# Kernel tuning notes

Measured on AMD Instinct MI355X. Metric: run time of the kernel, lower is better.

Reference implementation:

```python
import jax, jax.numpy as jnp
import numpy as np
import math

B, S, D = 1, 4096, 512
H, KVH, DH = 8, 4, 64
DH2 = DH // 2
M = int(math.isqrt(S))           # product-key grid side, S == M*M
K = 8                            # top_k
ROPE_BASE = 10000.0


def rope_cos_sin(seq_len, dh, base):
    inv_freq = 1.0 / (base ** (jnp.arange(0, dh, 2, dtype=jnp.float32) / dh))
    t = jnp.arange(seq_len, dtype=jnp.float32)
    freqs = jnp.outer(t, inv_freq)                      # (S, dh/2)
    emb = jnp.concatenate([freqs, freqs], axis=-1)      # (S, dh)
    return jnp.cos(emb), jnp.sin(emb)


def apply_rope(x, cos, sin):
    # x: (B, H, S, dh); half-split rotation (llama-style)
    dh2 = x.shape[-1] // 2
    rot = jnp.concatenate([-x[..., dh2:], x[..., :dh2]], axis=-1)
    return x * cos + rot * sin


def setup_inputs() -> dict:
    key = jax.random.key(0)
    ks = jax.random.split(key, 5)
    s = 0.02
    x = jax.random.normal(ks[0], (B, S, D), dtype=jnp.float32)
    Wq = jax.random.normal(ks[1], (H * DH, D), dtype=jnp.float32) * s
    Wk = jax.random.normal(ks[2], (KVH * DH, D), dtype=jnp.float32) * s
    Wv = jax.random.normal(ks[3], (KVH * DH, D), dtype=jnp.float32) * s
    Wo = jax.random.normal(ks[4], (D, H * DH), dtype=jnp.float32) * s
    return {"x": x, "Wq": Wq, "Wk": Wk, "Wv": Wv, "Wo": Wo}


def reference(x, Wq, Wk, Wv, Wo):
    b, s, d = x.shape
    cos, sin = rope_cos_sin(s, DH, ROPE_BASE)
    q = (x @ Wq.T).reshape(b, s, H, DH).transpose(0, 2, 1, 3)      # (B,H,S,DH)
    k = (x @ Wk.T).reshape(b, s, KVH, DH).transpose(0, 2, 1, 3)    # (B,KVH,S,DH)
    v = (x @ Wv.T).reshape(b, s, KVH, DH).transpose(0, 2, 1, 3)
    q = apply_rope(q, cos, sin)
    k = apply_rope(k, cos, sin)
    rep = H // KVH                                                 # GQA repeat_kv
    k = jnp.repeat(k, rep, axis=1)                                 # (B,H,S,DH)
    v = jnp.repeat(v, rep, axis=1)

    # factorized product keys: sum over grid rows / cols
    kg = k.reshape(b, H, M, M, DH)
    k1 = kg[..., :DH2].sum(axis=-2)                                # (B,H,M,DH2)
    k2 = kg[..., DH2:].sum(axis=-3)                                # (B,H,M,DH2)
    q1, q2 = q[..., :DH2], q[..., DH2:]

    def topk_sel(qh, kh):  # qh: (S,DH2), kh: (M,DH2)
        scores = qh @ kh.T                                         # (S,M)
        _, idx = jax.lax.top_k(scores, K)                          # (S,K)
        return kh[idx], idx                                        # (S,K,DH2), (S,K)

    sel2 = jax.vmap(jax.vmap(topk_sel))
    k1v, i1 = sel2(q1, k1)                                         # (B,H,S,K,DH2)
    k2v, i2 = sel2(q2, k2)

    # cross-product candidates: (B,H,S,K,K,DH) -> (B,H,S,K*K,DH)
    c1 = jnp.broadcast_to(k1v[:, :, :, :, None, :], (b, H, s, K, K, DH2))
    c2 = jnp.broadcast_to(k2v[:, :, :, None, :, :], (b, H, s, K, K, DH2))
    cand = jnp.concatenate([c1, c2], axis=-1).reshape(b, H, s, K * K, DH)

    scores_final = jnp.einsum('bhsd,bhscd->bhsc', q, cand)         # (B,H,S,K*K)
    _, sel = jax.lax.top_k(scores_final, K)                        # (B,H,S,K)
    final_k = jnp.take_along_axis(cand, sel[..., None], axis=3)    # (B,H,S,K,DH)

    row = jnp.take_along_axis(i1, sel // K, axis=3)
    col = jnp.take_along_axis(i2, sel % K, axis=3)
    v_idx = row * M + col                                          # (B,H,S,K)
    final_v = jax.vmap(jax.vmap(lambda vb, ib: vb[ib]))(v, v_idx)  # (B,H,S,K,DH)

    attn = jax.nn.softmax(
        jnp.einsum('bhsd,bhskd->bhsk', q, final_k) / math.sqrt(DH), axis=-1)
    o = jnp.einsum('bhsk,bhskd->bhsd', attn, final_v)              # (B,H,S,DH)
    o = o.transpose(0, 2, 1, 3).reshape(b, s, H * DH)
    return o @ Wo.T
```

## Files before the change

kernel.cpp:

```cpp
#include <hip/hip_runtime.h>
#include <math.h>


static constexpr size_t OFF_P1   = 0;
static constexpr size_t OFF_P2   = 4194304;
static constexpr size_t OFF_Q    = 8388608;
static constexpr size_t OFF_K    = 10485760;
static constexpr size_t OFF_V    = 11534336;
static constexpr size_t OFF_COS  = 12582912;
static constexpr size_t OFF_SIN  = 12713984;
static constexpr size_t OFF_K1   = 12845056;
static constexpr size_t OFF_K2   = 12853248;
static constexpr size_t OFF_O    = 12861440;
static constexpr size_t OFF_W    = 14958592;
static constexpr size_t OFF_PACK = 15482880;

#define LDB 132

__device__ __forceinline__ float rdlane_f(float v, int lane) {
  return __int_as_float(__builtin_amdgcn_readlane(__float_as_int(v), lane));
}

__global__ __launch_bounds__(256) void freq_table_kernel(float* __restrict__ cosT,
    float* __restrict__ sinT) {
  int idx = blockIdx.x * 256 + threadIdx.x;
  int s = idx >> 5;
  int dp = idx & 31;
  double e = (double)dp * (1.0 / 32.0);
  float pf = (float)pow(10000.0, e);
  float invf = 1.0f / pf;
  float argf = __fmul_rn((float)s, invf);
  cosT[idx] = (float)cos((double)argf);
  sinT[idx] = (float)sin((double)argf);
}

__global__ __launch_bounds__(256) void gemm128_panel(const float* __restrict__ A,
    const float* __restrict__ B, float* __restrict__ C1, float* __restrict__ C2,
    int N, int ksplit) {
  __shared__ float As[16 * LDB];
  __shared__ float Bs[16 * LDB];
  const int tid = threadIdx.x;
  const int z = blockIdx.z;
  const int k0 = z ? ksplit : 0;
  const int k1 = z ? 512 : ksplit;
  float* __restrict__ C = z ? C2 : C1;
  const int bm = blockIdx.y, bn = blockIdx.x;
  const int lrow = tid >> 1;
  const int lko = (tid & 1) << 3;
  const int ty = tid >> 4;
  const int tx = tid & 15;
  const float* Ap = A + (size_t)(bm * 128 + lrow) * 512 + lko;
  const float* Bp = B + (size_t)(bn * 128 + lrow) * 512 + lko;
  float acc[8][8] = {{0.f}};
  float4 a0 = *(const float4*)(Ap + k0);
  float4 a1 = *(const float4*)(Ap + k0 + 4);
  float4 b0 = *(const float4*)(Bp + k0);
  float4 b1 = *(const float4*)(Bp + k0 + 4);
  for (int kt = k0; kt < k1; kt += 16) {
    __syncthreads();
    As[(lko + 0) * LDB + lrow] = a0.x;
    As[(lko + 1) * LDB + lrow] = a0.y;
    As[(lko + 2) * LDB + lrow] = a0.z;
    As[(lko + 3) * LDB + lrow] = a0.w;
    As[(lko + 4) * LDB + lrow] = a1.x;
    As[(lko + 5) * LDB + lrow] = a1.y;
    As[(lko + 6) * LDB + lrow] = a1.z;
    As[(lko + 7) * LDB + lrow] = a1.w;
    Bs[(lko + 0) * LDB + lrow] = b0.x;
    Bs[(lko + 1) * LDB + lrow] = b0.y;
    Bs[(lko + 2) * LDB + lrow] = b0.z;
    Bs[(lko + 3) * LDB + lrow] = b0.w;
    Bs[(lko + 4) * LDB + lrow] = b1.x;
    Bs[(lko + 5) * LDB + lrow] = b1.y;
    Bs[(lko + 6) * LDB + lrow] = b1.z;
    Bs[(lko + 7) * LDB + lrow] = b1.w;
    __syncthreads();
    if (kt + 16 < k1) {
      a0 = *(const float4*)(Ap + kt + 16);
      a1 = *(const float4*)(Ap + kt + 20);
      b0 = *(const float4*)(Bp + kt + 16);
      b1 = *(const float4*)(Bp + kt + 20);
    }
    #pragma unroll
    for (int k = 0; k < 16; ++k) {
      float4 al = *(const float4*)(&As[k * LDB + (ty << 2)]);
      float4 ah = *(const float4*)(&As[k * LDB + 64 + (ty << 2)]);
      float4 bl = *(const float4*)(&Bs[k * LDB + (tx << 2)]);
      float4 bh = *(const float4*)(&Bs[k * LDB + 64 + (tx << 2)]);
      float af[8] = {al.x, al.y, al.z, al.w, ah.x, ah.y, ah.z, ah.w};
      float bf[8] = {bl.x, bl.y, bl.z, bl.w, bh.x, bh.y, bh.z, bh.w};
      #pragma unroll
      for (int i2 = 0; i2 < 8; ++i2)
        #pragma unroll
        for (int j2 = 0; j2 < 8; ++j2)
          acc[i2][j2] = fmaf(af[i2], bf[j2], acc[i2][j2]);
    }
  }
  #pragma unroll
  for (int i2 = 0; i2 < 8; ++i2) {
    int row = bm * 128 + ((i2 < 4) ? (ty << 2) + i2 : 64 + (ty << 2) + i2 - 4);
    float* Cp = C + (size_t)row * N + bn * 128;
    *(float4*)(Cp + (tx << 2))      = make_float4(acc[i2][0], acc[i2][1], acc[i2][2], acc[i2][3]);
    *(float4*)(Cp + 64 + (tx << 2)) = make_float4(acc[i2][4], acc[i2][5], acc[i2][6], acc[i2][7]);
  }
}

__global__ __launch_bounds__(256) void combine_kernel(const float* __restrict__ p1,
    const float* __restrict__ p2, float* __restrict__ out) {
  int i = blockIdx.x * 256 + threadIdx.x;
  out[i] = __fadd_rn(p1[i], p2[i]);
}

__global__ __launch_bounds__(256) void rope_reshape_kernel(const float* __restrict__ p1,
    const float* __restrict__ p2, const float* __restrict__ cosT,
    const float* __restrict__ sinT, float* __restrict__ qb,
    float* __restrict__ kb, float* __restrict__ vb) {
  int idx = blockIdx.x * 256 + threadIdx.x;
  int s = idx >> 10;
  int n = idx & 1023;
  float val = __fadd_rn(p1[idx], p2[idx]);
  int d = n & 63;
  if (n < 768) {
    int dp = d & 31;
    float cs = cosT[(s << 5) + dp];
    float sn = sinT[(s << 5) + dp];
    int npart = (n - d) + ((d < 32) ? d + 32 : d - 32);
    int pidx = (s << 10) + npart;
    float partner = __fadd_rn(p1[pidx], p2[pidx]);
    float rot = (d < 32) ? -partner : partner;
    float out = __fadd_rn(__fmul_rn(val, cs), __fmul_rn(rot, sn));
    if (n < 512) {
      int h = n >> 6;
      qb[((size_t)(h * 4096 + s) << 6) + d] = out;
    } else {
      int kvh = (n - 512) >> 6;
      kb[((size_t)(kvh * 4096 + s) << 6) + d] = out;
    }
  } else {
    int kvh = (n - 768) >> 6;
    vb[((size_t)(kvh * 4096 + s) << 6) + d] = val;
  }
}

__global__ __launch_bounds__(256) void k12_np_kernel(const float* __restrict__ kb,
    float* __restrict__ k1t, float* __restrict__ k2t) {
  int id = blockIdx.x * 256 + threadIdx.x;
  int which = id >> 13;
  int rem = id & 8191;
  int kvh = rem >> 11;
  int rem2 = rem & 2047;
  int i = rem2 >> 5;
  int d = rem2 & 31;
  const float* base = kb + ((size_t)(kvh * 4096) << 6);
  if (which == 0) {
    float acc = base[((size_t)(i * 64) << 6) + d];
    for (int c = 1; c < 64; ++c)
      acc = __fadd_rn(acc, base[((size_t)(i * 64 + c) << 6) + d]);
    k1t[(kvh * 64 + i) * 32 + d] = acc;
  } else {
    float acc = base[((size_t)i << 6) + d + 32];
    for (int r = 1; r < 64; ++r)
      acc = __fadd_rn(acc, base[((size_t)(r * 64 + i) << 6) + d + 32]);
    k2t[(kvh * 64 + i) * 32 + d] = acc;
  }
}

__global__ __launch_bounds__(256) void stage1_scoresT_kernel(
    const float* __restrict__ qb, const float* __restrict__ k1t,
    const float* __restrict__ k2t, float* __restrict__ scT) {
  __shared__ float qs[64 * 68];
  __shared__ float kd[32 * 132];
  const int t = threadIdx.x;
  const int h = blockIdx.y;
  const int s0 = blockIdx.x * 64;
  const int kvh = h >> 1;
  #pragma unroll
  for (int i = 0; i < 16; ++i) {
    int j = t + i * 256;
    int ss = j >> 6, d = j & 63;
    qs[d * 68 + ss] = qb[((size_t)(h * 4096 + s0 + ss) << 6) + d];
  }
  #pragma unroll
  for (int i = 0; i < 8; ++i) {
    int j = t + i * 256;
    int r = j >> 5, d = j & 31;
    kd[d * 132 + r]      = k1t[(kvh * 64 + r) * 32 + d];
    kd[d * 132 + 64 + r] = k2t[(kvh * 64 + r) * 32 + d];
  }
  __syncthreads();
  const int ty = t >> 4;
  const int tx = t & 15;
  float acc1[4][4] = {{0.f}};
  float acc2[4][4] = {{0.f}};
  #pragma unroll
  for (int dp = 0; dp < 32; ++dp) {
    float4 kv1 = *(const float4*)&kd[dp * 132 + (ty << 2)];
    float4 kv2 = *(const float4*)&kd[dp * 132 + 64 + (ty << 2)];
    float4 q1 = *(const float4*)&qs[dp * 68 + (tx << 2)];
    float4 q2 = *(const float4*)&qs[(32 + dp) * 68 + (tx << 2)];
    float k1f[4] = {kv1.x, kv1.y, kv1.z, kv1.w};
    float k2f[4] = {kv2.x, kv2.y, kv2.z, kv2.w};
    float q1f[4] = {q1.x, q1.y, q1.z, q1.w};
    float q2f[4] = {q2.x, q2.y, q2.z, q2.w};
    #pragma unroll
    for (int i2 = 0; i2 < 4; ++i2)
      #pragma unroll
      for (int j2 = 0; j2 < 4; ++j2) {
        acc1[i2][j2] = fmaf(k1f[i2], q1f[j2], acc1[i2][j2]);
        acc2[i2][j2] = fmaf(k2f[i2], q2f[j2], acc2[i2][j2]);
      }
  }
  float* base = scT + (size_t)h * 524288 + s0 + (tx << 2);
  #pragma unroll
  for (int i2 = 0; i2 < 4; ++i2) {
    *(float4*)(base + (size_t)((ty << 2) + i2) * 4096) =
        make_float4(acc1[i2][0], acc1[i2][1], acc1[i2][2], acc1[i2][3]);
    *(float4*)(base + (size_t)(64 + (ty << 2) + i2) * 4096) =
        make_float4(acc2[i2][0], acc2[i2][1], acc2[i2][2], acc2[i2][3]);
  }
}

__global__ __launch_bounds__(64) void sel1_kernel(const float* __restrict__ scT,
    ulonglong2* __restrict__ packs) {
  const int w = blockIdx.x * 64 + threadIdx.x;
  const int h = w >> 12;
  const int s = w & 4095;
  const float* base = scT + (size_t)h * 524288 + s;
  unsigned long long pk[2];
  #pragma unroll
  for (int set = 0; set < 2; ++set) {
    const float* p = base + (size_t)set * 64 * 4096;
    float top[8];
    int idx[8];
    #pragma unroll
    for (int t = 0; t < 8; ++t) { top[t] = -INFINITY; idx[t] = 0; }
    #pragma unroll
    for (int r = 0; r < 64; ++r) {
      float v = p[(size_t)r * 4096];
      int i = r;
      #pragma unroll
      for (int j = 0; j < 8; ++j) {
        bool gt = v > top[j];
        float tv = top[j]; int ti = idx[j];
        top[j] = gt ? v : tv;
        idx[j] = gt ? i : ti;
        v = gt ? tv : v;
        i = gt ? ti : i;
      }
    }
    unsigned long long pp = 0;
    #pragma unroll
    for (int t = 0; t < 8; ++t) pp |= (unsigned long long)idx[t] << (6 * t);
    pk[set] = pp;
  }
  ulonglong2 out;
  out.x = pk[0];
  out.y = pk[1];
  packs[w] = out;
}

__device__ __forceinline__ void bitonic64_val_desc(float& v, int lane) {
  #pragma unroll
  for (int k = 2; k <= 64; k <<= 1) {
    #pragma unroll
    for (int j = k >> 1; j >= 1; j >>= 1) {
      float ov = __shfl_xor(v, j, 64);
      bool up = ((lane & k) == 0) == ((lane & j) == 0);
      float mx = fmaxf(v, ov), mn = fminf(v, ov);
      v = up ? mx : mn;
    }
  }
}

__global__ __launch_bounds__(256) void attn_sel2_kernel(
    const ulonglong2* __restrict__ packs, const float* __restrict__ qb,
    const float* __restrict__ vb, const float* __restrict__ k1t,
    const float* __restrict__ k2t, float* __restrict__ ob) {
  const int lane = threadIdx.x & 63;
  const int w = blockIdx.x * 4 + (threadIdx.x >> 6);
  const int h = w >> 12;
  const int s = w & 4095;
  const int kvh = h >> 1;
  ulonglong2 pk = packs[w];
  const unsigned long long pack1 = pk.x, pack2 = pk.y;
  const float qv = qb[((size_t)w << 6) + lane];

  int r1 = (int)((pack1 >> (6 * (lane >> 3))) & 63);
  int r2 = (int)((pack2 >> (6 * (lane & 7))) & 63);
  const float* k1p = k1t + (size_t)(kvh * 64 + r1) * 32;
  const float* k2p = k2t + (size_t)(kvh * 64 + r2) * 32;
  float c = 0.f;
  #pragma unroll
  for (int dq = 0; dq < 32; dq += 4) {
    float4 kk = *(const float4*)(k1p + dq);
    c = __fadd_rn(c, __fmul_rn(rdlane_f(qv, dq + 0), kk.x));
    c = __fadd_rn(c, __fmul_rn(rdlane_f(qv, dq + 1), kk.y));
    c = __fadd_rn(c, __fmul_rn(rdlane_f(qv, dq + 2), kk.z));
    c = __fadd_rn(c, __fmul_rn(rdlane_f(qv, dq + 3), kk.w));
  }
  #pragma unroll
  for (int dq = 0; dq < 32; dq += 4) {
    float4 kk = *(const float4*)(k2p + dq);
    c = __fadd_rn(c, __fmul_rn(rdlane_f(qv, 32 + dq + 0), kk.x));
    c = __fadd_rn(c, __fmul_rn(rdlane_f(qv, 32 + dq + 1), kk.y));
    c = __fadd_rn(c, __fmul_rn(rdlane_f(qv, 32 + dq + 2), kk.z));
    c = __fadd_rn(c, __fmul_rn(rdlane_f(qv, 32 + dq + 3), kk.w));
  }
  const float scand = c;
  float v3 = c;
  bitonic64_val_desc(v3, lane);
  float cvs[8]; int ccs[8];
  unsigned long long used = 0;
  #pragma unroll
  for (int t = 0; t < 8; ++t) {
    float tv = rdlane_f(v3, t);
    unsigned long long m = __ballot(scand == tv) & ~used;
    int ix = __ffsll((long long)m) - 1;
    used |= 1ull << ix;
    cvs[t] = tv;
    ccs[t] = ix;
  }
  float y[8];
  #pragma unroll
  for (int t = 0; t < 8; ++t) y[t] = cvs[t] * 0.125f;
  float mx = y[0];
  #pragma unroll
  for (int t = 1; t < 8; ++t) if (y[t] > mx) mx = y[t];
  float e[8];
  #pragma unroll
  for (int t = 0; t < 8; ++t) e[t] = __expf(__fsub_rn(y[t], mx));
  float wsum = __fadd_rn(__fadd_rn(__fadd_rn(e[0], e[1]), __fadd_rn(e[2], e[3])),
                         __fadd_rn(__fadd_rn(e[4], e[5]), __fadd_rn(e[6], e[7])));
  const float* vbh = vb + ((size_t)kvh << 18);
  float o = 0.f;
  #pragma unroll
  for (int t = 0; t < 8; ++t) {
    float att = __fdiv_rn(e[t], wsum);
    int row = (int)((pack1 >> (6 * (ccs[t] >> 3))) & 63);
    int col = (int)((pack2 >> (6 * (ccs[t] & 7))) & 63);
    o = __fadd_rn(o, __fmul_rn(att, vbh[((size_t)(row * 64 + col) << 6) + lane]));
  }
  ob[(size_t)s * 512 + (h << 6) + lane] = o;
}

extern "C" void kernel_launch(void* const* d_in, const int* in_sizes, int n_in,
                              void* d_out, int out_size, void* d_ws, size_t ws_size,
                              hipStream_t stream) {
  const float* x  = (const float*)d_in[0];
  const float* Wq = (const float*)d_in[1];
  const float* Wk = (const float*)d_in[2];
  const float* Wv = (const float*)d_in[3];
  const float* Wo = (const float*)d_in[4];
  float* ws = (float*)d_ws;
  float* p1   = ws + OFF_P1;
  float* p2   = ws + OFF_P2;
  float* qb   = ws + OFF_Q;
  float* kb   = ws + OFF_K;
  float* vb   = ws + OFF_V;
  float* cosT = ws + OFF_COS;
  float* sinT = ws + OFF_SIN;
  float* k1t  = ws + OFF_K1;
  float* k2t  = ws + OFF_K2;
  float* ob   = ws + OFF_O;
  float* wcat = ws + OFF_W;
  float* scT  = ws + OFF_P1;
  float* op1  = ws + OFF_P2;
  float* op2  = ws + OFF_P2 + 2097152;
  ulonglong2* packs = (ulonglong2*)(ws + OFF_PACK);

  hipMemcpyAsync(wcat,             Wq, (size_t)512 * 512 * sizeof(float), hipMemcpyDeviceToDevice, stream);
  hipMemcpyAsync(wcat + 512 * 512, Wk, (size_t)256 * 512 * sizeof(float), hipMemcpyDeviceToDevice, stream);
  hipMemcpyAsync(wcat + 768 * 512, Wv, (size_t)256 * 512 * sizeof(float), hipMemcpyDeviceToDevice, stream);

  freq_table_kernel<<<512, 256, 0, stream>>>(cosT, sinT);
  gemm128_panel<<<dim3(8, 32, 2), 256, 0, stream>>>(x, wcat, p1, p2, 1024, 384);
  rope_reshape_kernel<<<16384, 256, 0, stream>>>(p1, p2, cosT, sinT, qb, kb, vb);
  k12_np_kernel<<<64, 256, 0, stream>>>(kb, k1t, k2t);
  stage1_scoresT_kernel<<<dim3(64, 8), 256, 0, stream>>>(qb, k1t, k2t, scT);
  sel1_kernel<<<512, 64, 0, stream>>>(scT, packs);
  attn_sel2_kernel<<<8192, 256, 0, stream>>>(packs, qb, vb, k1t, k2t, ob);
  gemm128_panel<<<dim3(4, 32, 2), 256, 0, stream>>>(ob, Wo, op1, op2, 512, 256);
  combine_kernel<<<8192, 256, 0, stream>>>(op1, op2, (float*)d_out);
}
```

Measured before the change: 256.7 us.

## Fuse stage-1 top-k selection into score kernel and drop weight concat copies

The stage-1 score kernel now stages its 128x64 score tile in shared memory and runs the per-query top-8 selection in the same block, so the separate selection kernel and the global score buffer round trip go away. A new QKV GEMM variant reads Wq, Wk and Wv directly through per-block base pointers, which removes the three device-to-device memcpys that built a concatenated weight matrix. As a trade-off, only 128 of 256 threads do the selection inside the fused kernel, and shared memory is reused across phases.

Result: faster. 241.6 us (-5.9%).

```diff
diff --git a/kernel.cpp b/kernel.cpp
--- a/kernel.cpp
+++ b/kernel.cpp
@@ -12,8 +12,7 @@
 static constexpr size_t OFF_K1   = 12845056;
 static constexpr size_t OFF_K2   = 12853248;
 static constexpr size_t OFF_O    = 12861440;
-static constexpr size_t OFF_W    = 14958592;
-static constexpr size_t OFF_PACK = 15482880;
+static constexpr size_t OFF_PACK = 14958592;
 
 #define LDB 132
 
@@ -32,6 +31,81 @@
   float argf = __fmul_rn((float)s, invf);
   cosT[idx] = (float)cos((double)argf);
   sinT[idx] = (float)sin((double)argf);
+}
+
+__global__ __launch_bounds__(256) void gemm128_qkv(const float* __restrict__ A,
+    const float* __restrict__ Wq, const float* __restrict__ Wk,
+    const float* __restrict__ Wv, float* __restrict__ C1,
+    float* __restrict__ C2) {
+  __shared__ float As[16 * LDB];
+  __shared__ float Bs[16 * LDB];
+  const int tid = threadIdx.x;
+  const int z = blockIdx.z;
+  const int k0 = z ? 384 : 0;
+  const int k1 = z ? 512 : 384;
+  float* __restrict__ C = z ? C2 : C1;
+  const int bm = blockIdx.y, bn = blockIdx.x;
+  const int lrow = tid >> 1;
+  const int lko = (tid & 1) << 3;
+  const int ty = tid >> 4;
+  const int tx = tid & 15;
+  const float* Bbase = (bn < 4) ? (Wq + ((size_t)bn * 128) * 512)
+                     : (bn < 6) ? (Wk + ((size_t)(bn - 4) * 128) * 512)
+                                : (Wv + ((size_t)(bn - 6) * 128) * 512);
+  const float* Ap = A + (size_t)(bm * 128 + lrow) * 512 + lko;
+  const float* Bp = Bbase + (size_t)lrow * 512 + lko;
+  float acc[8][8] = {{0.f}};
+  float4 a0 = *(const float4*)(Ap + k0);
+  float4 a1 = *(const float4*)(Ap + k0 + 4);
+  float4 b0 = *(const float4*)(Bp + k0);
+  float4 b1 = *(const float4*)(Bp + k0 + 4);
+  for (int kt = k0; kt < k1; kt += 16) {
+    __syncthreads();
+    As[(lko + 0) * LDB + lrow] = a0.x;
+    As[(lko + 1) * LDB + lrow] = a0.y;
+    As[(lko + 2) * LDB + lrow] = a0.z;
+    As[(lko + 3) * LDB + lrow] = a0.w;
+    As[(lko + 4) * LDB + lrow] = a1.x;
+    As[(lko + 5) * LDB + lrow] = a1.y;
+    As[(lko + 6) * LDB + lrow] = a1.z;
+    As[(lko + 7) * LDB + lrow] = a1.w;
+    Bs[(lko + 0) * LDB + lrow] = b0.x;
+    Bs[(lko + 1) * LDB + lrow] = b0.y;
+    Bs[(lko + 2) * LDB + lrow] = b0.z;
+    Bs[(lko + 3) * LDB + lrow] = b0.w;
+    Bs[(lko + 4) * LDB + lrow] = b1.x;
+    Bs[(lko + 5) * LDB + lrow] = b1.y;
+    Bs[(lko + 6) * LDB + lrow] = b1.z;
+    Bs[(lko + 7) * LDB + lrow] = b1.w;
+    __syncthreads();
+    if (kt + 16 < k1) {
+      a0 = *(const float4*)(Ap + kt + 16);
+      a1 = *(const float4*)(Ap + kt + 20);
+      b0 = *(const float4*)(Bp + kt + 16);
+      b1 = *(const float4*)(Bp + kt + 20);
+    }
+    #pragma unroll
+    for (int k = 0; k < 16; ++k) {
+      float4 al = *(const float4*)(&As[k * LDB + (ty << 2)]);
+      float4 ah = *(const float4*)(&As[k * LDB + 64 + (ty << 2)]);
+      float4 bl = *(const float4*)(&Bs[k * LDB + (tx << 2)]);
+      float4 bh = *(const float4*)(&Bs[k * LDB + 64 + (tx << 2)]);
+      float af[8] = {al.x, al.y, al.z, al.w, ah.x, ah.y, ah.z, ah.w};
+      float bf[8] = {bl.x, bl.y, bl.z, bl.w, bh.x, bh.y, bh.z, bh.w};
+      #pragma unroll
+      for (int i2 = 0; i2 < 8; ++i2)
+        #pragma unroll
+        for (int j2 = 0; j2 < 8; ++j2)
+          acc[i2][j2] = fmaf(af[i2], bf[j2], acc[i2][j2]);
+    }
+  }
+  #pragma unroll
+  for (int i2 = 0; i2 < 8; ++i2) {
+    int row = bm * 128 + ((i2 < 4) ? (ty << 2) + i2 : 64 + (ty << 2) + i2 - 4);
+    float* Cp = C + (size_t)row * 1024 + bn * 128;
+    *(float4*)(Cp + (tx << 2))      = make_float4(acc[i2][0], acc[i2][1], acc[i2][2], acc[i2][3]);
+    *(float4*)(Cp + 64 + (tx << 2)) = make_float4(acc[i2][4], acc[i2][5], acc[i2][6], acc[i2][7]);
+  }
 }
 
 __global__ __launch_bounds__(256) void gemm128_panel(const float* __restrict__ A,
@@ -165,11 +239,12 @@
   }
 }
 
-__global__ __launch_bounds__(256) void stage1_scoresT_kernel(
+__global__ __launch_bounds__(256) void stage1_sel_kernel(
     const float* __restrict__ qb, const float* __restrict__ k1t,
-    const float* __restrict__ k2t, float* __restrict__ scT) {
-  __shared__ float qs[64 * 68];
-  __shared__ float kd[32 * 132];
+    const float* __restrict__ k2t, unsigned long long* __restrict__ packs) {
+  __shared__ float smem[8704];
+  float* qs = smem;
+  float* kd = smem + 4352;
   const int t = threadIdx.x;
   const int h = blockIdx.y;
   const int s0 = blockIdx.x * 64;
@@ -210,33 +285,28 @@
         acc2[i2][j2] = fmaf(k2f[i2], q2f[j2], acc2[i2][j2]);
       }
   }
-  float* base = scT + (size_t)h * 524288 + s0 + (tx << 2);
+  __syncthreads();
+  float* sct = smem;
   #pragma unroll
   for (int i2 = 0; i2 < 4; ++i2) {
-    *(float4*)(base + (size_t)((ty << 2) + i2) * 4096) =
+    int r = (ty << 2) + i2;
+    *(float4*)&sct[(size_t)r * 68 + (tx << 2)] =
         make_float4(acc1[i2][0], acc1[i2][1], acc1[i2][2], acc1[i2][3]);
-    *(float4*)(base + (size_t)(64 + (ty << 2) + i2) * 4096) =
+    *(float4*)&sct[(size_t)(64 + r) * 68 + (tx << 2)] =
         make_float4(acc2[i2][0], acc2[i2][1], acc2[i2][2], acc2[i2][3]);
   }
-}
-
-__global__ __launch_bounds__(64) void sel1_kernel(const float* __restrict__ scT,
-    ulonglong2* __restrict__ packs) {
-  const int w = blockIdx.x * 64 + threadIdx.x;
-  const int h = w >> 12;
-  const int s = w & 4095;
-  const float* base = scT + (size_t)h * 524288 + s;
-  unsigned long long pk[2];
-  #pragma unroll
-  for (int set = 0; set < 2; ++set) {
-    const float* p = base + (size_t)set * 64 * 4096;
+  __syncthreads();
+  if (t < 128) {
+    int set = t >> 6;
+    int sq = t & 63;
+    const float* p = sct + (size_t)(set << 6) * 68 + sq;
     float top[8];
     int idx[8];
     #pragma unroll
-    for (int t = 0; t < 8; ++t) { top[t] = -INFINITY; idx[t] = 0; }
+    for (int u = 0; u < 8; ++u) { top[u] = -INFINITY; idx[u] = 0; }
     #pragma unroll
     for (int r = 0; r < 64; ++r) {
-      float v = p[(size_t)r * 4096];
+      float v = p[(size_t)r * 68];
       int i = r;
       #pragma unroll
       for (int j = 0; j < 8; ++j) {
@@ -250,13 +320,9 @@
     }
     unsigned long long pp = 0;
     #pragma unroll
-    for (int t = 0; t < 8; ++t) pp |= (unsigned long long)idx[t] << (6 * t);
-    pk[set] = pp;
-  }
-  ulonglong2 out;
-  out.x = pk[0];
-  out.y = pk[1];
-  packs[w] = out;
+    for (int u = 0; u < 8; ++u) pp |= (unsigned long long)idx[u] << (6 * u);
+    packs[(((size_t)(h * 4096 + s0 + sq)) << 1) + set] = pp;
+  }
 }
 
 __device__ __forceinline__ void bitonic64_val_desc(float& v, int lane) {
@@ -362,23 +428,16 @@
   float* k1t  = ws + OFF_K1;
   float* k2t  = ws + OFF_K2;
   float* ob   = ws + OFF_O;
-  float* wcat = ws + OFF_W;
-  float* scT  = ws + OFF_P1;
   float* op1  = ws + OFF_P2;
   float* op2  = ws + OFF_P2 + 2097152;
-  ulonglong2* packs = (ulonglong2*)(ws + OFF_PACK);
-
-  hipMemcpyAsync(wcat,             Wq, (size_t)512 * 512 * sizeof(float), hipMemcpyDeviceToDevice, stream);
-  hipMemcpyAsync(wcat + 512 * 512, Wk, (size_t)256 * 512 * sizeof(float), hipMemcpyDeviceToDevice, stream);
-  hipMemcpyAsync(wcat + 768 * 512, Wv, (size_t)256 * 512 * sizeof(float), hipMemcpyDeviceToDevice, stream);
+  unsigned long long* packs = (unsigned long long*)(ws + OFF_PACK);
 
   freq_table_kernel<<<512, 256, 0, stream>>>(cosT, sinT);
-  gemm128_panel<<<dim3(8, 32, 2), 256, 0, stream>>>(x, wcat, p1, p2, 1024, 384);
+  gemm128_qkv<<<dim3(8, 32, 2), 256, 0, stream>>>(x, Wq, Wk, Wv, p1, p2);
   rope_reshape_kernel<<<16384, 256, 0, stream>>>(p1, p2, cosT, sinT, qb, kb, vb);
   k12_np_kernel<<<64, 256, 0, stream>>>(kb, k1t, k2t);
-  stage1_scoresT_kernel<<<dim3(64, 8), 256, 0, stream>>>(qb, k1t, k2t, scT);
-  sel1_kernel<<<512, 64, 0, stream>>>(scT, packs);
-  attn_sel2_kernel<<<8192, 256, 0, stream>>>(packs, qb, vb, k1t, k2t, ob);
+  stage1_sel_kernel<<<dim3(64, 8), 256, 0, stream>>>(qb, k1t, k2t, packs);
+  attn_sel2_kernel<<<8192, 256, 0, stream>>>((const ulonglong2*)packs, qb, vb, k1t, k2t, ob);
   gemm128_panel<<<dim3(4, 32, 2), 256, 0, stream>>>(ob, Wo, op1, op2, 512, 256);
   combine_kernel<<<8192, 256, 0, stream>>>(op1, op2, (float*)d_out);
 }
```
